# Performance work log

Hardware: AMD Instinct MI355X
Metric: run time of the kernel (lower is better)

The kernel has to match this reference:

```python
import jax, jax.numpy as jnp
import numpy as np

B, T, D, C = 2, 2048, 1024, 10
F = D // 2 + 1  # rfft bins; permutations act on frequency bins (perm_freq=True)


def setup_inputs() -> dict:
    key = jax.random.key(0)
    ks = jax.random.split(key, 6)
    s = 1.0 / np.sqrt(D)
    x = jax.random.normal(ks[0], (B, T, D), jnp.float32)
    Wq = jax.random.normal(ks[1], (D, D), jnp.float32) * s
    Wk = jax.random.normal(ks[2], (D, D), jnp.float32) * s
    Wv = jax.random.normal(ks[3], (D, D), jnp.float32) * s
    Wo = jax.random.normal(ks[4], (D, D), jnp.float32) * s
    # buffer: torch.randn(C, F).argsort(-1) -> random permutations of freq bins
    perms = jnp.argsort(jax.random.normal(ks[5], (C, F)), axis=-1)
    return {"x": x, "Wq": Wq, "Wk": Wk, "Wv": Wv, "Wo": Wo, "perms": perms}


def reference(x, Wq, Wk, Wv, Wo, perms):
    # linear projections (nn.Linear applies x @ W.T)
    q = x @ Wq.T
    k = x @ Wk.T
    v = x @ Wv.T
    # HRR bind/unbind in rfft frequency domain
    fq = jnp.fft.rfft(q, axis=-1)  # (B,T,F) complex
    fk = jnp.fft.rfft(k, axis=-1)
    fv = jnp.fft.rfft(v, axis=-1)
    # gather permuted redundant copies of freq bins: (B,T,C,F) -> (C,B,T,F)
    fkp = jnp.moveaxis(fk[..., perms], 2, 0)
    fqp = jnp.moveaxis(fq[..., perms], 2, 0)
    # causal associative memory: cumulative sum of key*value bindings over time
    kv = jnp.cumsum(fkp * fv[None], axis=-2)  # (C,B,T,F)
    # unbind with query (circular correlation = multiply by conj), mean copies
    r = jnp.mean(kv * jnp.conj(fqp), axis=0)  # (B,T,F)
    values_hat = jnp.fft.irfft(r, n=D, axis=-1)  # (B,T,D)
    return values_hat @ Wo.T
```

## Files before the change

kernel.cpp:

```cpp
#include <hip/hip_runtime.h>
#include <math.h>

#define B_   2
#define T_   2048
#define D_   1024
#define C_   10
#define F_   513
#define NTOK (B_ * T_)
#define LF   3078
#define LFP  3136
#define KP2  1056
#define NCH  128
#define TC   (T_ / NCH)

typedef unsigned short us16;
typedef __attribute__((ext_vector_type(8))) __bf16 bf16x8;
typedef __attribute__((ext_vector_type(4))) float  f32x4;

#define O_XBF    ((size_t)0)
#define O_PREP   ((size_t)8388608)
#define O_WT     (O_PREP)
#define O_WOBF   (O_PREP + 6291456)
#define O_TCS    (O_PREP + 8388608)
#define O_RCAT   (O_PREP)
#define O_SFB    (O_PREP + 10489856)
#define O_MALLB  (O_SFB + 2162688)
#define O_MOUTB  (O_MALLB + 6303744)
#define O_FALL   (O_MOUTB + 2162688)
#define O_SSCAN  (O_FALL + 25690112)

__device__ __forceinline__ us16 f2b(float f) {
    union { float f; unsigned u; } v; v.f = f;
    unsigned r = v.u + 0x7FFFu + ((v.u >> 16) & 1u);
    return (us16)(r >> 16);
}

__device__ __forceinline__ float2 b2f2(unsigned w) {
    union { unsigned u; float f; } a, b;
    a.u = (w & 0xffffu) << 16;
    b.u = w & 0xffff0000u;
    return make_float2(a.f, b.f);
}

__device__ __forceinline__ void gl_lds16(const us16* g, us16* l) {
    __builtin_amdgcn_global_load_lds(
        (const __attribute__((address_space(1))) unsigned*)g,
        (__attribute__((address_space(3))) unsigned*)l, 16, 0, 0);
}

__global__ __launch_bounds__(256)
void hrr_prep(const float* __restrict__ x,  const float* __restrict__ Wq,
              const float* __restrict__ Wk, const float* __restrict__ Wv,
              const float* __restrict__ Wo,
              us16* __restrict__ Xbf, us16* __restrict__ WT,
              us16* __restrict__ WoBf, us16* __restrict__ Tcs,
              us16* __restrict__ Sfb) {
    __shared__ float t[32][33];
    const int bid = blockIdx.x, tid = threadIdx.x;
    if (bid < 4096) {
        int i = bid * 256 + tid;
        float4 v = ((const float4*)x)[i];
        ushort4 o;
        o.x = f2b(v.x); o.y = f2b(v.y); o.z = f2b(v.z); o.w = f2b(v.w);
        ((ushort4*)Xbf)[i] = o;
    } else if (bid < 5120) {
        int i = (bid - 4096) * 256 + tid;
        float4 v = ((const float4*)Wo)[i];
        ushort4 o;
        o.x = f2b(v.x); o.y = f2b(v.y); o.z = f2b(v.z); o.w = f2b(v.w);
        ((ushort4*)WoBf)[i] = o;
    } else if (bid < 8192) {
        const int l  = bid - 5120;
        const int bz = l >> 10, l2 = l & 1023;
        const int bx = (l2 & 31) * 32, by = (l2 >> 5) * 32;
        const float* W = (bz == 0) ? Wq : (bz == 1) ? Wk : Wv;
        us16* O = WT + (size_t)bz * D_ * D_;
        const int tx = tid & 31, ty = tid >> 5;
#pragma unroll
        for (int i = 0; i < 32; i += 8)
            t[ty + i][tx] = W[(size_t)(by + ty + i) * D_ + bx + tx];
        __syncthreads();
#pragma unroll
        for (int i = 0; i < 32; i += 8)
            O[(size_t)(bx + ty + i) * D_ + by + tx] = f2b(t[tx][ty + i]);
    } else if (bid < 12296) {
        int idx = (bid - 8192) * 256 + tid;
        int r = idx >> 10, e = idx & 1023;
        int f = r >> 1;
        float ang = (float)((f * e) & 1023) * 6.135923151542565e-3f;
        Tcs[idx] = f2b((r & 1) ? -sinf(ang) : cosf(ang));
    } else {
        int idx = (bid - 12296) * 256 + tid;
        int r = idx >> 10, e = idx & 1023;
        float v = 0.f;
        if (r < 1026) {
            int f = r >> 1;
            float s = (f == 0 || f == 512) ? (1.0f / 1024.0f) : (2.0f / 1024.0f);
            float ang = (float)((f * e) & 1023) * 6.135923151542565e-3f;
            v = (r & 1) ? -s * sinf(ang) : s * cosf(ang);
        }
        Sfb[idx] = f2b(v);
    }
}

template <bool OUT_BF16>
__device__ __forceinline__ void gemm_core(
    const us16* __restrict__ A, const us16* __restrict__ B, void* __restrict__ Cv,
    int M, int N, int K, int lda, int ldb, int ldc, int Ncap,
    int bm, int bn, us16* smem) {
    us16* As = smem;
    us16* Bs = smem + 8192;

    const int tid  = threadIdx.x;
    const int lane = tid & 63;
    const int wave = tid >> 6;
    const int wm = (wave >> 1) * 64;
    const int wn = (wave & 1) * 64;

    const int r0    = tid >> 2;
    const int g_lds = tid & 3;
    const int g_src = g_lds ^ ((r0 >> 1) & 3);
    const int c4    = g_src * 8;

    int rA0 = bm + r0;      if (rA0 >= M) rA0 = M - 1;
    int rA1 = bm + 64 + r0; if (rA1 >= M) rA1 = M - 1;
    int rB0 = bn + r0;      if (rB0 >= N) rB0 = N - 1;
    int rB1 = bn + 64 + r0; if (rB1 >= N) rB1 = N - 1;
    const us16* pA0 = A + (size_t)rA0 * lda + c4;
    const us16* pA1 = A + (size_t)rA1 * lda + c4;
    const us16* pB0 = B + (size_t)rB0 * ldb + c4;
    const us16* pB1 = B + (size_t)rB1 * ldb + c4;

    f32x4 acc[4][4];
#pragma unroll
    for (int i = 0; i < 4; i++)
#pragma unroll
        for (int j = 0; j < 4; j++) acc[i][j] = (f32x4){0.f, 0.f, 0.f, 0.f};

    const int fr = lane & 15;
    const int gq = ((lane >> 4) ^ ((fr >> 1) & 3)) * 8;

    const int wb = wave * 512;
#define STAGE_TILE(buf, ko)                                  \
    do {                                                     \
        us16* a_ = As + (buf) * 4096 + wb;                   \
        us16* b_ = Bs + (buf) * 4096 + wb;                   \
        gl_lds16(pA0 + (ko), a_);                            \
        gl_lds16(pA1 + (ko), a_ + 2048);                     \
        gl_lds16(pB0 + (ko), b_);                            \
        gl_lds16(pB1 + (ko), b_ + 2048);                     \
    } while (0)

    STAGE_TILE(0, 0);
    __syncthreads();

    int cur = 0;
    for (int k0 = 0; k0 < K; k0 += 32) {
        const int kn = k0 + 32;
        if (kn < K) STAGE_TILE(cur ^ 1, kn);

        const us16* Ac = As + cur * 4096;
        const us16* Bc = Bs + cur * 4096;
        bf16x8 af[4], bfr[4];
#pragma unroll
        for (int i = 0; i < 4; i++)
            af[i] = *(const bf16x8*)(Ac + (wm + i * 16 + fr) * 32 + gq);
#pragma unroll
        for (int j = 0; j < 4; j++)
            bfr[j] = *(const bf16x8*)(Bc + (wn + j * 16 + fr) * 32 + gq);
#pragma unroll
        for (int i = 0; i < 4; i++)
#pragma unroll
            for (int j = 0; j < 4; j++)
                acc[i][j] = __builtin_amdgcn_mfma_f32_16x16x32_bf16(bfr[j], af[i], acc[i][j], 0, 0, 0);

        __syncthreads();
        cur ^= 1;
    }
#undef STAGE_TILE

    const int cl  = lane & 15;
    const int rq  = (lane >> 4) * 4;
    float* lbuf = (float*)smem;
#pragma unroll
    for (int p = 0; p < 4; ++p) {
        __syncthreads();
        if ((wave >> 1) == (p >> 1)) {
            const int ib = (p & 1) * 2;
#pragma unroll
            for (int ii = 0; ii < 2; ++ii) {
                const int rl = ii * 16 + cl;
#pragma unroll
                for (int j = 0; j < 4; ++j)
                    *(f32x4*)(lbuf + rl * 132 + wn + j * 16 + rq) = acc[ib + ii][j];
            }
        }
        __syncthreads();
        const int rbase = bm + p * 32;
        if (OUT_BF16) {
            us16* C = (us16*)Cv;
#pragma unroll
            for (int rr = 0; rr < 2; ++rr) {
                const int idx = rr * 2048 + tid * 8;
                const int row = idx >> 7, col = idx & 127;
                const int grow = rbase + row, gcol = bn + col;
                if (grow < M && gcol + 8 <= Ncap) {
                    const float* s = lbuf + row * 132 + col;
                    uint4 o;
                    o.x = (unsigned)f2b(s[0]) | ((unsigned)f2b(s[1]) << 16);
                    o.y = (unsigned)f2b(s[2]) | ((unsigned)f2b(s[3]) << 16);
                    o.z = (unsigned)f2b(s[4]) | ((unsigned)f2b(s[5]) << 16);
                    o.w = (unsigned)f2b(s[6]) | ((unsigned)f2b(s[7]) << 16);
                    *(uint4*)(C + (size_t)grow * ldc + gcol) = o;
                }
            }
        } else {
            float* C = (float*)Cv;
#pragma unroll
            for (int rr = 0; rr < 4; ++rr) {
                const int idx = rr * 1024 + tid * 4;
                const int row = idx >> 7, col = idx & 127;
                const int grow = rbase + row, gcol = bn + col;
                if (grow < M && gcol + 4 <= Ncap)
                    *(float4*)(C + (size_t)grow * ldc + gcol) =
                        *(const float4*)(lbuf + row * 132 + col);
            }
        }
    }
}

template <bool OUT_BF16>
__global__ __launch_bounds__(256, 3)
void hrr_gemm(const us16* __restrict__ A, const us16* __restrict__ B,
              void* __restrict__ C, int M, int N, int K,
              int lda, int ldb, int ldc, int Ncap, int swz) {
    __shared__ us16 smem[16384];
    int bx = blockIdx.x, by = blockIdx.y;
    if (swz) {
        const int gx = gridDim.x;
        const int id = bx + gx * by;
        const int q = (gx * gridDim.y) >> 3;
        const int nid = (id & 7) * q + (id >> 3);
        bx = nid % gx; by = nid / gx;
    }
    gemm_core<OUT_BF16>(A, B, C, M, N, K, lda, ldb, ldc, Ncap,
                        by * 128, bx * 128, smem);
}

__global__ __launch_bounds__(256, 3)
void hrr_gemm_builders(const us16* __restrict__ Tcs, const us16* __restrict__ WT,
                       us16* __restrict__ MallB, const us16* __restrict__ WoBf,
                       const us16* __restrict__ Sfb, us16* __restrict__ MoutB) {
    __shared__ us16 smem[16384];
    const int bm = blockIdx.y * 128, bn = blockIdx.x * 128;
    const int z = blockIdx.z;
    if (z < 3)
        gemm_core<true>(Tcs, WT + (size_t)z * D_ * D_,
                        MallB + (size_t)z * 1026 * 1024,
                        1026, 1024, 1024, 1024, 1024, 1024, 1024, bm, bn, smem);
    else
        gemm_core<true>(WoBf, Sfb, MoutB,
                        1024, KP2, 1024, 1024, 1024, KP2, KP2, bm, bn, smem);
}

__global__ __launch_bounds__(512, 2)
void hrr_gemm_main(const us16* __restrict__ A, const us16* __restrict__ B,
                   us16* __restrict__ C) {
    __shared__ us16 smem[65536];
    us16* Asb = smem;
    us16* Bsb = smem + 32768;

    const int tid  = threadIdx.x;
    const int lane = tid & 63;
    const int wave = tid >> 6;

    int id = blockIdx.x + 13 * blockIdx.y;
    id = (id & 7) * 26 + (id >> 3);
    const int bx = id % 13, by = id / 13;
    const int bm = by * 256, bn = bx * 256;

    const int srow = tid >> 3;
    const int sgr  = (tid & 7) ^ (srow & 7);
    const us16* gA[4];
    const us16* gB[4];
#pragma unroll
    for (int g = 0; g < 4; ++g) {
        int ra = bm + g * 64 + srow; if (ra > NTOK - 1) ra = NTOK - 1;
        int rb = bn + g * 64 + srow; if (rb > LF - 1)   rb = LF - 1;
        gA[g] = A + (size_t)ra * 1024 + sgr * 8;
        gB[g] = B + (size_t)rb * 1024 + sgr * 8;
    }

    f32x4 acc[8][4];
#pragma unroll
    for (int i = 0; i < 8; i++)
#pragma unroll
        for (int j = 0; j < 4; j++) acc[i][j] = (f32x4){0.f, 0.f, 0.f, 0.f};

    const int wmw = (wave >> 2) * 128;
    const int wnw = (wave & 3) * 64;
    const int fr  = lane & 15;
    const int gr  = lane >> 4;
    const int l7  = lane & 7;

#define STAGE3(buf, ko)                                            \
    do {                                                           \
        us16* a_ = Asb + (buf) * 16384 + wave * 512;               \
        us16* b_ = Bsb + (buf) * 16384 + wave * 512;               \
        gl_lds16(gA[0] + (ko), a_);                                \
        gl_lds16(gA[1] + (ko), a_ + 4096);                         \
        gl_lds16(gA[2] + (ko), a_ + 8192);                         \
        gl_lds16(gA[3] + (ko), a_ + 12288);                        \
        gl_lds16(gB[0] + (ko), b_);                                \
        gl_lds16(gB[1] + (ko), b_ + 4096);                         \
        gl_lds16(gB[2] + (ko), b_ + 8192);                         \
        gl_lds16(gB[3] + (ko), b_ + 12288);                        \
    } while (0)

#define RBAR                                                       \
    do {                                                           \
        asm volatile("" ::: "memory");                             \
        __builtin_amdgcn_s_barrier();                              \
        asm volatile("" ::: "memory");                             \
    } while (0)

#define LOAD_A(ih)                                                              \
    do {                                                                        \
        _Pragma("unroll")                                                       \
        for (int i = 0; i < 4; ++i)                                             \
            _Pragma("unroll")                                                   \
            for (int ks = 0; ks < 2; ++ks)                                      \
                af[i][ks] = *(const bf16x8*)(Ac +                               \
                    (wmw + (ih) * 64 + i * 16 + fr) * 64 +                      \
                    (((ks << 2) | gr) ^ l7) * 8);                               \
    } while (0)

#define LOAD_B(jh)                                                              \
    do {                                                                        \
        _Pragma("unroll")                                                       \
        for (int j = 0; j < 2; ++j)                                             \
            _Pragma("unroll")                                                   \
            for (int ks = 0; ks < 2; ++ks)                                      \
                bfr[j][ks] = *(const bf16x8*)(Bc +                              \
                    (wnw + (jh) * 32 + j * 16 + fr) * 64 +                      \
                    (((ks << 2) | gr) ^ l7) * 8);                               \
    } while (0)

#define MFMA_Q(ih, jh)                                                          \
    do {                                                                        \
        __builtin_amdgcn_s_setprio(1);                                          \
        _Pragma("unroll")                                                       \
        for (int i = 0; i < 4; ++i)                                             \
            _Pragma("unroll")                                                   \
            for (int j = 0; j < 2; ++j)                                         \
                _Pragma("unroll")                                               \
                for (int ks = 0; ks < 2; ++ks)                                  \
                    acc[(ih) * 4 + i][(jh) * 2 + j] =                           \
                        __builtin_amdgcn_mfma_f32_16x16x32_bf16(                \
                            bfr[j][ks], af[i][ks],                              \
                            acc[(ih) * 4 + i][(jh) * 2 + j], 0, 0, 0);          \
        __builtin_amdgcn_s_setprio(0);                                          \
    } while (0)

    STAGE3(0, 0);
    asm volatile("s_waitcnt vmcnt(0)" ::: "memory");
    __builtin_amdgcn_s_barrier();
    asm volatile("" ::: "memory");

    int cur = 0;
#pragma unroll 1
    for (int t = 0; t < 16; ++t) {
        if (t < 15) STAGE3(cur ^ 1, (t + 1) * 64);

        const us16* Ac = Asb + cur * 16384;
        const us16* Bc = Bsb + cur * 16384;
        bf16x8 af[4][2], bfr[2][2];

        LOAD_A(0); LOAD_B(0); MFMA_Q(0, 0); RBAR;
        LOAD_B(1);            MFMA_Q(0, 1); RBAR;
        LOAD_A(1);            MFMA_Q(1, 1); RBAR;
        LOAD_B(0);            MFMA_Q(1, 0);
        asm volatile("s_waitcnt vmcnt(0)" ::: "memory");
        __builtin_amdgcn_s_barrier();
        asm volatile("" ::: "memory");
        cur ^= 1;
    }
#undef STAGE3
#undef LOAD_A
#undef LOAD_B
#undef MFMA_Q
#undef RBAR

    __syncthreads();
    float* lw = (float*)smem + wave * (32 * 68);
    const int cl = lane & 15;
    const int rq = (lane >> 4) * 4;
#pragma unroll
    for (int p = 0; p < 4; ++p) {
#pragma unroll
        for (int ii = 0; ii < 2; ++ii) {
            const int ifr = p * 2 + ii;
#pragma unroll
            for (int j = 0; j < 4; ++j)
                *(f32x4*)(lw + (ii * 16 + cl) * 68 + j * 16 + rq) = acc[ifr][j];
        }
        __syncthreads();
#pragma unroll
        for (int rr = 0; rr < 4; ++rr) {
            const int idx = rr * 512 + lane * 8;
            const int row = idx >> 6, col = idx & 63;
            const int grow = bm + wmw + p * 32 + row;
            const int gcol = bn + wnw + col;
            if (gcol + 8 <= LFP) {
                const float* s = lw + row * 68 + col;
                uint4 o;
                o.x = (unsigned)f2b(s[0]) | ((unsigned)f2b(s[1]) << 16);
                o.y = (unsigned)f2b(s[2]) | ((unsigned)f2b(s[3]) << 16);
                o.z = (unsigned)f2b(s[4]) | ((unsigned)f2b(s[5]) << 16);
                o.w = (unsigned)f2b(s[6]) | ((unsigned)f2b(s[7]) << 16);
                *(uint4*)(C + (size_t)grow * LFP + gcol) = o;
            }
        }
        __syncthreads();
    }
}

__global__ __launch_bounds__(256, 4)
void hrr_scan_sums(const us16* __restrict__ Fall, const int* __restrict__ perms,
                   float* __restrict__ S) {
    const int n = blockIdx.x, b = blockIdx.y, half = blockIdx.z;
    const int tid = threadIdx.x;
    const int f0 = half * 256;
    const int VL = half ? 257 : 256;
    __shared__ float2 kc[F_], vc[257];

    float aR[2][C_], aI[2][C_];
    int gg[2][C_];
#pragma unroll
    for (int i = 0; i < 2; i++) {
        const int f = (i == 0) ? (f0 + tid) : 512;
        const bool act = (i == 0) || (half == 1 && tid == 0);
#pragma unroll
        for (int c = 0; c < C_; c++) {
            gg[i][c] = act ? perms[c * F_ + f] : 0;
            aR[i][c] = aI[i][c] = 0.f;
        }
    }

    for (int tl = 0; tl < TC; tl++) {
        const us16* row = Fall + (size_t)(b * T_ + n * TC + tl) * LFP;
        __syncthreads();
        for (int j = tid; j < F_; j += 256)
            kc[j] = b2f2(*(const unsigned*)(row + 1026 + 2 * j));
        for (int j = tid; j < VL; j += 256)
            vc[j] = b2f2(*(const unsigned*)(row + 2052 + 2 * (f0 + j)));
        __syncthreads();
#pragma unroll
        for (int i = 0; i < 2; i++) {
            const int lv = (i == 0) ? tid : 256;
            if (i == 0 || (half == 1 && tid == 0)) {
                float2 v = vc[lv];
#pragma unroll
                for (int c = 0; c < C_; c++) {
                    float2 k = kc[gg[i][c]];
                    aR[i][c] += k.x * v.x - k.y * v.y;
                    aI[i][c] += k.x * v.y + k.y * v.x;
                }
            }
        }
    }
#pragma unroll
    for (int i = 0; i < 2; i++) {
        const int f = (i == 0) ? (f0 + tid) : 512;
        if (i == 0 || (half == 1 && tid == 0)) {
#pragma unroll
            for (int c = 0; c < C_; c++) {
                size_t a = ((((size_t)c * B_ + b) * NCH + n) * F_ + f) * 2;
                S[a] = aR[i][c]; S[a + 1] = aI[i][c];
            }
        }
    }
}

__global__ void hrr_scan_prefix(float* __restrict__ S) {
    int tid = blockIdx.x * 256 + threadIdx.x;
    if (tid >= C_ * B_ * F_) return;
    int c = tid / (B_ * F_);
    int r = tid % (B_ * F_);
    int b = r / F_, f = r % F_;
    size_t base = (((size_t)c * B_ + b) * NCH) * F_ + f;
    float runR = 0.f, runI = 0.f;
    for (int n0 = 0; n0 < NCH; n0 += 8) {
        float tR[8], tI[8];
#pragma unroll
        for (int u = 0; u < 8; u++) {
            size_t a = (base + (size_t)(n0 + u) * F_) * 2;
            tR[u] = S[a]; tI[u] = S[a + 1];
        }
#pragma unroll
        for (int u = 0; u < 8; u++) {
            size_t a = (base + (size_t)(n0 + u) * F_) * 2;
            S[a] = runR; S[a + 1] = runI;
            runR += tR[u]; runI += tI[u];
        }
    }
}

__global__ __launch_bounds__(256, 4)
void hrr_scan_apply(const us16* __restrict__ Fall, const int* __restrict__ perms,
                    const float* __restrict__ S, us16* __restrict__ Rcat) {
    const int n = blockIdx.x, b = blockIdx.y, half = blockIdx.z;
    const int tid = threadIdx.x;
    const int f0 = half * 256;
    const int VL = half ? 257 : 256;
    __shared__ float2 qc[F_], kc[F_], vc[257];

    float kvR[2][C_], kvI[2][C_];
    int gg[2][C_];
#pragma unroll
    for (int i = 0; i < 2; i++) {
        const int f = (i == 0) ? (f0 + tid) : 512;
        const bool act = (i == 0) || (half == 1 && tid == 0);
#pragma unroll
        for (int c = 0; c < C_; c++) {
            gg[i][c] = act ? perms[c * F_ + f] : 0;
            if (act) {
                size_t a = ((((size_t)c * B_ + b) * NCH + n) * F_ + f) * 2;
                kvR[i][c] = S[a]; kvI[i][c] = S[a + 1];
            } else { kvR[i][c] = 0.f; kvI[i][c] = 0.f; }
        }
    }

    for (int tl = 0; tl < TC; tl++) {
        const int tt = b * T_ + n * TC + tl;
        const us16* row = Fall + (size_t)tt * LFP;
        __syncthreads();
        for (int j = tid; j < F_; j += 256) {
            qc[j] = b2f2(*(const unsigned*)(row + 2 * j));
            kc[j] = b2f2(*(const unsigned*)(row + 1026 + 2 * j));
        }
        for (int j = tid; j < VL; j += 256)
            vc[j] = b2f2(*(const unsigned*)(row + 2052 + 2 * (f0 + j)));
        __syncthreads();
        unsigned* out32 = (unsigned*)(Rcat + (size_t)tt * KP2);
#pragma unroll
        for (int i = 0; i < 2; i++) {
            const int f = (i == 0) ? (f0 + tid) : 512;
            const int lv = (i == 0) ? tid : 256;
            if (i == 0 || (half == 1 && tid == 0)) {
                float2 v = vc[lv];
                float accR = 0.f, accI = 0.f;
#pragma unroll
                for (int c = 0; c < C_; c++) {
                    int g = gg[i][c];
                    float2 k = kc[g];
                    float nR = kvR[i][c] + k.x * v.x - k.y * v.y;
                    float nI = kvI[i][c] + k.x * v.y + k.y * v.x;
                    kvR[i][c] = nR; kvI[i][c] = nI;
                    float2 q = qc[g];
                    accR += nR * q.x + nI * q.y;
                    accI += nI * q.x - nR * q.y;
                }
                out32[f] = (unsigned)f2b(accR * 0.1f)
                         | ((unsigned)f2b(accI * 0.1f) << 16);
            }
        }
        if (half == 0 && tid < 15)
            out32[513 + tid] = 0;
    }
}

extern "C" void kernel_launch(void* const* d_in, const int* in_sizes, int n_in,
                              void* d_out, int out_size, void* d_ws, size_t ws_size,
                              hipStream_t stream) {
    const float* x  = (const float*)d_in[0];
    const float* Wq = (const float*)d_in[1];
    const float* Wk = (const float*)d_in[2];
    const float* Wv = (const float*)d_in[3];
    const float* Wo = (const float*)d_in[4];
    const int* perms = (const int*)d_in[5];
    float* out = (float*)d_out;

    char* ws = (char*)d_ws;
    us16* Xbf   = (us16*)(ws + O_XBF);
    us16* WT    = (us16*)(ws + O_WT);
    us16* WoBf  = (us16*)(ws + O_WOBF);
    us16* Tcs   = (us16*)(ws + O_TCS);
    us16* Sfb   = (us16*)(ws + O_SFB);
    us16* MallB = (us16*)(ws + O_MALLB);
    us16* MoutB = (us16*)(ws + O_MOUTB);
    us16* Rcat  = (us16*)(ws + O_RCAT);
    us16* Fall  = (us16*)(ws + O_FALL);
    float* Ssc  = (float*)(ws + O_SSCAN);

    hrr_prep<<<16520, 256, 0, stream>>>(x, Wq, Wk, Wv, Wo, Xbf, WT, WoBf, Tcs, Sfb);

    hrr_gemm_builders<<<dim3(9, 9, 4), 256, 0, stream>>>(Tcs, WT, MallB, WoBf, Sfb, MoutB);

    hrr_gemm_main<<<dim3(13, 16), 512, 0, stream>>>(Xbf, MallB, Fall);

    hrr_scan_sums<<<dim3(NCH, B_, 2), 256, 0, stream>>>(Fall, perms, Ssc);
    hrr_scan_prefix<<<(C_ * B_ * F_ + 255) / 256, 256, 0, stream>>>(Ssc);
    hrr_scan_apply<<<dim3(NCH, B_, 2), 256, 0, stream>>>(Fall, perms, Ssc, Rcat);

    hrr_gemm<false><<<dim3(8, 32), 256, 0, stream>>>(
        Rcat, MoutB, out, NTOK, D_, KP2, KP2, KP2, D_, D_, 1);
}
```

Baseline: 237.7 us.

## Pad spectral row layout for vector loads and double scan chunk count

Realigns the K and V sections of each fused spectrum row to 8-byte boundaries (offsets 1028/2056, MROWS 1028) so the scan kernels can stage q/k/v bins with uint2 loads instead of strided scalar loops. It also doubles the number of time chunks in the chunked scan, which raises block-level parallelism in the sum and apply passes at the cost of a longer cross-chunk prefix pass. The builder GEMM output and buffer offsets are resized to match the padded layout.

```diff
diff --git a/kernel.cpp b/kernel.cpp
--- a/kernel.cpp
+++ b/kernel.cpp
@@ -7,10 +7,13 @@
 #define C_   10
 #define F_   513
 #define NTOK (B_ * T_)
-#define LF   3078
+#define KOFF 1028
+#define VOFF 2056
+#define LFU  3082
 #define LFP  3136
+#define MROWS 1028
 #define KP2  1056
-#define NCH  128
+#define NCH  256
 #define TC   (T_ / NCH)
 
 typedef unsigned short us16;
@@ -25,7 +28,7 @@
 #define O_RCAT   (O_PREP)
 #define O_SFB    (O_PREP + 10489856)
 #define O_MALLB  (O_SFB + 2162688)
-#define O_MOUTB  (O_MALLB + 6303744)
+#define O_MOUTB  (O_MALLB + 6316032)
 #define O_FALL   (O_MOUTB + 2162688)
 #define O_SSCAN  (O_FALL + 25690112)
 
@@ -167,7 +170,7 @@
             af[i] = *(const bf16x8*)(Ac + (wm + i * 16 + fr) * 32 + gq);
 #pragma unroll
         for (int j = 0; j < 4; j++)
-            bfr[j] = *(const bf16x8*)(Bc + (wn + j * 16 + fr) * 32 + gq);
+            bfr[j] = *(const bf16x8*)(Bs + cur * 4096 + (wn + j * 16 + fr) * 32 + gq);
 #pragma unroll
         for (int i = 0; i < 4; i++)
 #pragma unroll
@@ -176,6 +179,7 @@
 
         __syncthreads();
         cur ^= 1;
+        (void)Bc;
     }
 #undef STAGE_TILE
 
@@ -256,7 +260,7 @@
     const int z = blockIdx.z;
     if (z < 3)
         gemm_core<true>(Tcs, WT + (size_t)z * D_ * D_,
-                        MallB + (size_t)z * 1026 * 1024,
+                        MallB + (size_t)z * MROWS * 1024,
                         1026, 1024, 1024, 1024, 1024, 1024, 1024, bm, bn, smem);
     else
         gemm_core<true>(WoBf, Sfb, MoutB,
@@ -286,7 +290,7 @@
 #pragma unroll
     for (int g = 0; g < 4; ++g) {
         int ra = bm + g * 64 + srow; if (ra > NTOK - 1) ra = NTOK - 1;
-        int rb = bn + g * 64 + srow; if (rb > LF - 1)   rb = LF - 1;
+        int rb = bn + g * 64 + srow; if (rb > LFU - 1)  rb = LFU - 1;
         gA[g] = A + (size_t)ra * 1024 + sgr * 8;
         gB[g] = B + (size_t)rb * 1024 + sgr * 8;
     }
@@ -431,7 +435,6 @@
     const int n = blockIdx.x, b = blockIdx.y, half = blockIdx.z;
     const int tid = threadIdx.x;
     const int f0 = half * 256;
-    const int VL = half ? 257 : 256;
     __shared__ float2 kc[F_], vc[257];
 
     float aR[2][C_], aI[2][C_];
@@ -448,12 +451,23 @@
     }
 
     for (int tl = 0; tl < TC; tl++) {
-        const us16* row = Fall + (size_t)(b * T_ + n * TC + tl) * LFP;
-        __syncthreads();
-        for (int j = tid; j < F_; j += 256)
-            kc[j] = b2f2(*(const unsigned*)(row + 1026 + 2 * j));
-        for (int j = tid; j < VL; j += 256)
-            vc[j] = b2f2(*(const unsigned*)(row + 2052 + 2 * (f0 + j)));
+        const unsigned* row32 =
+            (const unsigned*)(Fall + (size_t)(b * T_ + n * TC + tl) * LFP);
+        __syncthreads();
+        {
+            uint2 kk = *(const uint2*)(row32 + 514 + 2 * tid);
+            kc[2 * tid]     = b2f2(kk.x);
+            kc[2 * tid + 1] = b2f2(kk.y);
+            if (tid < 128) {
+                uint2 vv = *(const uint2*)(row32 + 1028 + f0 + 2 * tid);
+                vc[2 * tid]     = b2f2(vv.x);
+                vc[2 * tid + 1] = b2f2(vv.y);
+            }
+            if (tid == 0) {
+                kc[512] = b2f2(row32[1026]);
+                if (half == 1) vc[256] = b2f2(row32[1540]);
+            }
+        }
         __syncthreads();
 #pragma unroll
         for (int i = 0; i < 2; i++) {
@@ -512,7 +526,6 @@
     const int n = blockIdx.x, b = blockIdx.y, half = blockIdx.z;
     const int tid = threadIdx.x;
     const int f0 = half * 256;
-    const int VL = half ? 257 : 256;
     __shared__ float2 qc[F_], kc[F_], vc[257];
 
     float kvR[2][C_], kvI[2][C_];
@@ -533,14 +546,26 @@
 
     for (int tl = 0; tl < TC; tl++) {
         const int tt = b * T_ + n * TC + tl;
-        const us16* row = Fall + (size_t)tt * LFP;
-        __syncthreads();
-        for (int j = tid; j < F_; j += 256) {
-            qc[j] = b2f2(*(const unsigned*)(row + 2 * j));
-            kc[j] = b2f2(*(const unsigned*)(row + 1026 + 2 * j));
-        }
-        for (int j = tid; j < VL; j += 256)
-            vc[j] = b2f2(*(const unsigned*)(row + 2052 + 2 * (f0 + j)));
+        const unsigned* row32 = (const unsigned*)(Fall + (size_t)tt * LFP);
+        __syncthreads();
+        {
+            uint2 qq = *(const uint2*)(row32 + 2 * tid);
+            qc[2 * tid]     = b2f2(qq.x);
+            qc[2 * tid + 1] = b2f2(qq.y);
+            uint2 kk = *(const uint2*)(row32 + 514 + 2 * tid);
+            kc[2 * tid]     = b2f2(kk.x);
+            kc[2 * tid + 1] = b2f2(kk.y);
+            if (tid < 128) {
+                uint2 vv = *(const uint2*)(row32 + 1028 + f0 + 2 * tid);
+                vc[2 * tid]     = b2f2(vv.x);
+                vc[2 * tid + 1] = b2f2(vv.y);
+            }
+            if (tid == 0) {
+                qc[512] = b2f2(row32[512]);
+                kc[512] = b2f2(row32[1026]);
+                if (half == 1) vc[256] = b2f2(row32[1540]);
+            }
+        }
         __syncthreads();
         unsigned* out32 = (unsigned*)(Rcat + (size_t)tt * KP2);
 #pragma unroll
```

After: 248.4 us. +4.5%, slower.
